# Kernel optimization log

Hardware: AMD Instinct MI355X
Metric: run time of the kernel (lower is better)

## Reference

```python
import jax, jax.numpy as jnp
import numpy as np

N_NODES = 100000
N_EDGES = 1600000
IN_DIM = 128
OUT_DIM = 64
N_HEADS = 4
NEG_SLOPE = 0.2
EPS = 1e-8


def setup_inputs() -> dict:
    key = jax.random.key(0)
    ks = jax.random.split(key, 6)
    x = jax.random.normal(ks[0], (N_NODES, IN_DIM), dtype=jnp.float32)
    edge_index = jax.random.randint(ks[1], (2, N_EDGES), 0, N_NODES, dtype=jnp.int64)
    # Xavier-uniform-ish init for linear weights, torch layout [out, in]
    bound = float(np.sqrt(6.0 / (IN_DIM + OUT_DIM)))
    Wq = jax.random.uniform(ks[2], (N_HEADS, OUT_DIM, IN_DIM), jnp.float32, -bound, bound)
    Wk = jax.random.uniform(ks[3], (N_HEADS, OUT_DIM, IN_DIM), jnp.float32, -bound, bound)
    Wh = jax.random.uniform(ks[4], (N_HEADS, OUT_DIM, IN_DIM), jnp.float32, -bound, bound)
    bh = jax.random.uniform(ks[5], (N_HEADS, OUT_DIM), jnp.float32, -bound, bound)
    return {"x": x, "edge_index": edge_index, "Wq": Wq, "Wk": Wk, "Wh": Wh, "bh": bh}


def reference(x, edge_index, Wq, Wk, Wh, bh):
    n_nodes = x.shape[0]
    row, col = edge_index[0], edge_index[1]
    n_heads = Wq.shape[0]
    scale = Wq.shape[1] ** 0.5
    outs = []
    for h in range(n_heads):  # fixed small head count; params differ per head
        Q = x @ Wq[h].T                                   # [N, out]
        K = x @ Wk[h].T                                   # [N, out]
        q_i = jax.nn.leaky_relu(Q[row], NEG_SLOPE)        # [E, out]
        k_j = jax.nn.leaky_relu(K[col], NEG_SLOPE)        # [E, out]
        scores = jnp.sum(q_i * k_j, axis=1) / scale       # [E]
        m = jax.ops.segment_max(scores, row, num_segments=n_nodes)
        e = jnp.exp(scores - m[row])
        z = jax.ops.segment_sum(e, row, num_segments=n_nodes)
        alpha = e / (z[row] + EPS)                        # [E]
        h_j = (x @ Wh[h].T + bh[h])[col]                  # [E, out]
        outs.append(jax.ops.segment_sum(alpha[:, None] * h_j, row, num_segments=n_nodes))
    return jnp.mean(jnp.stack(outs, axis=0), axis=0)      # [N, out]
```

## Files before the change

kernel.cpp:

```cpp
#include <hip/hip_runtime.h>
#include <math.h>

#define NIN 128
#define NOUT 64
#define FEAT 256
#define KHROW 512

typedef __attribute__((ext_vector_type(8))) short short8;
typedef __attribute__((ext_vector_type(4))) float f32x4;

__device__ __forceinline__ unsigned short f2bf(float f) {
    unsigned u = __float_as_uint(f);
    u = (u + 0x7FFFu + ((u >> 16) & 1u)) >> 16;
    return (unsigned short)u;
}
__device__ __forceinline__ float bflo(unsigned u) {
    return __uint_as_float(u << 16);
}
__device__ __forceinline__ float bfhi(unsigned u) {
    return __uint_as_float(u & 0xffff0000u);
}

__global__ __launch_bounds__(256) void wconv_kernel(
    const float* __restrict__ Wq, const float* __restrict__ Wk,
    const float* __restrict__ Wh, unsigned short* __restrict__ Wsw)
{
    const int id = blockIdx.x * 256 + threadIdx.x;
    const int lane = id & 63;
    const int kb   = (id >> 6) & 3;
    const int tile = (id >> 8) & 3;
    const int head = (id >> 10) & 3;
    const int mat  = id >> 12;
    const float* src = (mat == 0) ? Wq : (mat == 1) ? Wk : Wh;
    const int row   = tile * 16 + (lane & 15);
    const int kbase = kb * 32 + (lane >> 4) * 8;
    const float* sp = src + (size_t)(head * 64 + row) * NIN + kbase;
    const float4 a = *(const float4*)sp;
    const float4 b = *(const float4*)(sp + 4);
    uint4 w;
    w.x = (unsigned)f2bf(a.x) | ((unsigned)f2bf(a.y) << 16);
    w.y = (unsigned)f2bf(a.z) | ((unsigned)f2bf(a.w) << 16);
    w.z = (unsigned)f2bf(b.x) | ((unsigned)f2bf(b.y) << 16);
    w.w = (unsigned)f2bf(b.z) | ((unsigned)f2bf(b.w) << 16);
    *(uint4*)(Wsw + (size_t)id * 8) = w;
}

__global__ __launch_bounds__(256) void gemm_mfma_kernel(
    const float* __restrict__ x, const unsigned short* __restrict__ Wsw,
    const float* __restrict__ bh,
    unsigned short* __restrict__ QL, unsigned short* __restrict__ KH, int N,
    const int* __restrict__ ei, int E, int* __restrict__ deg,
    int* __restrict__ epos, int GB)
{
    if (blockIdx.x >= GB) {
        for (int e = (blockIdx.x - GB) * 256 + threadIdx.x; e < E; e += 512 * 256)
            epos[e] = atomicAdd(&deg[ei[e]], 1);
        return;
    }

    __shared__ char smem[34816];
    unsigned short (*xs)[136] = (unsigned short (*)[136])smem;

    const int nb = blockIdx.x * 128;
    const int t  = threadIdx.x;
    const int w  = t >> 6;
    const int l  = t & 63;

    #pragma unroll
    for (int j = 0; j < 16; ++j) {
        const int idx = j * 256 + t;
        const int row = idx >> 5;
        const int c4  = idx & 31;
        float4 xv = make_float4(0.f, 0.f, 0.f, 0.f);
        if (nb + row < N)
            xv = *(const float4*)(x + (size_t)(nb + row) * NIN + c4 * 4);
        ushort4 pk;
        pk.x = f2bf(xv.x); pk.y = f2bf(xv.y); pk.z = f2bf(xv.z); pk.w = f2bf(xv.w);
        *(ushort4*)(&xs[row][c4 * 4]) = pk;
    }
    __syncthreads();

    short8 bfrx[2][4];
    #pragma unroll
    for (int ns = 0; ns < 2; ++ns)
        #pragma unroll
        for (int kb = 0; kb < 4; ++kb)
            bfrx[ns][kb] = *(const short8*)(
                &xs[w * 32 + ns * 16 + (l & 15)][kb * 32 + (l >> 4) * 8]);
    __syncthreads();

    char* const sbw = smem + w * 4608;
    unsigned short* const wl = (unsigned short*)(smem + 18432);
    const int fsub = (l >> 4) * 4;

    for (int g = 0; g < 12; ++g) {
        const int mat  = g >> 2;
        const int head = g & 3;

        {
            const uint4* gw = (const uint4*)(Wsw + (size_t)g * 8192);
            uint4* wl4 = (uint4*)wl;
            #pragma unroll
            for (int j = 0; j < 4; ++j)
                wl4[j * 256 + t] = gw[j * 256 + t];
        }
        __syncthreads();

        #pragma unroll
        for (int tile = 0; tile < 4; ++tile) {
            f32x4 a0 = (f32x4){0.f, 0.f, 0.f, 0.f};
            f32x4 a1 = (f32x4){0.f, 0.f, 0.f, 0.f};
            #pragma unroll
            for (int kb = 0; kb < 4; ++kb) {
                const short8 afrw = *(const short8*)(
                    wl + (((tile * 4 + kb) << 9) + (l << 3)));
                a0 = __builtin_amdgcn_mfma_f32_16x16x32_bf16(afrw, bfrx[0][kb], a0, 0, 0, 0);
                a1 = __builtin_amdgcn_mfma_f32_16x16x32_bf16(afrw, bfrx[1][kb], a1, 0, 0, 0);
            }
            #pragma unroll
            for (int ns = 0; ns < 2; ++ns) {
                const f32x4 av = ns ? a1 : a0;
                float v0 = av[0], v1 = av[1], v2 = av[2], v3 = av[3];
                const int node = (l & 15) + ns * 16;
                if (mat == 2) {
                    const float4 bv = *(const float4*)(bh + head * NOUT + tile * 16 + fsub);
                    v0 += bv.x; v1 += bv.y; v2 += bv.z; v3 += bv.w;
                } else {
                    v0 = (v0 > 0.f) ? v0 : 0.2f * v0;
                    v1 = (v1 > 0.f) ? v1 : 0.2f * v1;
                    v2 = (v2 > 0.f) ? v2 : 0.2f * v2;
                    v3 = (v3 > 0.f) ? v3 : 0.2f * v3;
                }
                uint2 pk;
                pk.x = (unsigned)f2bf(v0) | ((unsigned)f2bf(v1) << 16);
                pk.y = (unsigned)f2bf(v2) | ((unsigned)f2bf(v3) << 16);
                *(uint2*)(sbw + node * 144 + (tile * 16 + fsub) * 2) = pk;
            }
        }

        #pragma unroll
        for (int jj = 0; jj < 4; ++jj) {
            const int node  = (l >> 3) + jj * 8;
            const int gnode = nb + w * 32 + node;
            const uint4 v = *(const uint4*)(sbw + node * 144 + (l & 7) * 16);
            if (gnode < N) {
                char* ob;
                if (mat == 0)      ob = (char*)QL + (size_t)gnode * 512 + head * 128;
                else if (mat == 1) ob = (char*)KH + (size_t)gnode * 1024 + head * 128;
                else               ob = (char*)KH + (size_t)gnode * 1024 + 512 + head * 128;
                *(uint4*)(ob + (l & 7) * 16) = v;
            }
        }
        __syncthreads();
    }
}

__global__ __launch_bounds__(1024) void bsum_kernel(const int* __restrict__ deg, int N,
                                                    int* __restrict__ bsum)
{
    __shared__ int wsum[16];
    const int t = threadIdx.x;
    const int idx = blockIdx.x * 1024 + t;
    int v = (idx < N) ? deg[idx] : 0;
    #pragma unroll
    for (int off = 1; off < 64; off <<= 1) v += __shfl_xor(v, off);
    if ((t & 63) == 0) wsum[t >> 6] = v;
    __syncthreads();
    if (t < 16) {
        int s = wsum[t];
        #pragma unroll
        for (int off = 1; off < 16; off <<= 1) s += __shfl_xor(s, off);
        if (t == 0) bsum[blockIdx.x] = s;
    }
}

__global__ __launch_bounds__(1024) void bscan_kernel(int* __restrict__ bsum, int NB,
                                                     int* __restrict__ rowstart, int N)
{
    __shared__ int wsum[16];
    const int t = threadIdx.x, lane = t & 63, wid = t >> 6;
    const int v = (t < NB) ? bsum[t] : 0;
    int s = v;
    #pragma unroll
    for (int off = 1; off < 64; off <<= 1) {
        int u = __shfl_up(s, off);
        if (lane >= off) s += u;
    }
    if (lane == 63) wsum[wid] = s;
    __syncthreads();
    if (wid == 0 && lane < 16) {
        int ss = wsum[lane];
        #pragma unroll
        for (int off = 1; off < 16; off <<= 1) {
            int u = __shfl_up(ss, off);
            if (lane >= off) ss += u;
        }
        wsum[lane] = ss;
    }
    __syncthreads();
    const int woff = (wid == 0) ? 0 : wsum[wid - 1];
    if (t < NB) bsum[t] = s + woff - v;
    if (t == 1023) rowstart[N] = s + woff;
}

__global__ __launch_bounds__(1024) void scan_apply_kernel(
    const int* __restrict__ deg, const int* __restrict__ bsum, int N,
    int* __restrict__ rowstart)
{
    __shared__ int wsum[16];
    const int t = threadIdx.x, lane = t & 63, wid = t >> 6;
    const int idx = blockIdx.x * 1024 + t;
    const int v = (idx < N) ? deg[idx] : 0;
    int s = v;
    #pragma unroll
    for (int off = 1; off < 64; off <<= 1) {
        int u = __shfl_up(s, off);
        if (lane >= off) s += u;
    }
    if (lane == 63) wsum[wid] = s;
    __syncthreads();
    if (wid == 0 && lane < 16) {
        int ss = wsum[lane];
        #pragma unroll
        for (int off = 1; off < 16; off <<= 1) {
            int u = __shfl_up(ss, off);
            if (lane >= off) ss += u;
        }
        wsum[lane] = ss;
    }
    __syncthreads();
    const int woff = (wid == 0) ? 0 : wsum[wid - 1];
    if (idx < N) rowstart[idx] = s + woff - v + bsum[blockIdx.x];
}

__global__ __launch_bounds__(256) void fill_kernel(const int* __restrict__ ei, int E,
                                                   const int* __restrict__ rowstart,
                                                   const int* __restrict__ epos,
                                                   int* __restrict__ csr_col)
{
    const int e = blockIdx.x * 256 + threadIdx.x;
    if (e < E)
        csr_col[rowstart[ei[e]] + epos[e]] = ei[E + e];
}

__global__ __launch_bounds__(256) void attn_kernel(
    const unsigned short* __restrict__ QL, const unsigned short* __restrict__ KH,
    const int* __restrict__ rowstart, const int* __restrict__ csr_col,
    float* __restrict__ out, int base, int N)
{
    const int n = base + blockIdx.x * 4 + (threadIdx.x >> 6);
    if (n >= N) return;
    const int l  = threadIdx.x & 63;
    const int g  = l >> 4;
    const int koff = ((l >> 2) & 3) * 64 + (l & 3) * 16;

    float qf[16];
    {
        const uint4* qp = (const uint4*)(QL + (size_t)n * FEAT + koff);
        const uint4 q0 = qp[0], q1 = qp[1];
        unsigned qs[8] = {q0.x, q0.y, q0.z, q0.w, q1.x, q1.y, q1.z, q1.w};
        #pragma unroll
        for (int tt = 0; tt < 8; ++tt) {
            qf[2 * tt]     = bflo(qs[tt]);
            qf[2 * tt + 1] = bfhi(qs[tt]);
        }
    }

    const int s0 = rowstart[n];
    const int s1 = rowstart[n + 1];

    float acc[16];
    #pragma unroll
    for (int j = 0; j < 16; ++j) acc[j] = 0.f;
    float z = 0.f;

    for (int i = s0; i < s1; i += 4) {
        const int eidx = i + g;
        if (eidx < s1) {
            const int c = csr_col[eidx];
            const uint4* kp = (const uint4*)(KH + (size_t)c * KHROW + koff);
            const uint4 k0 = kp[0],  k1 = kp[1];
            const uint4 h0 = kp[32], h1 = kp[33];

            unsigned ks[8] = {k0.x, k0.y, k0.z, k0.w, k1.x, k1.y, k1.z, k1.w};
            float p = 0.f;
            #pragma unroll
            for (int tt = 0; tt < 8; ++tt) {
                p = fmaf(qf[2 * tt],     bflo(ks[tt]), p);
                p = fmaf(qf[2 * tt + 1], bfhi(ks[tt]), p);
            }
            p += __shfl_xor(p, 1);
            p += __shfl_xor(p, 2);

            const float e = __expf(p * 0.125f);
            z += e;
            unsigned hs[8] = {h0.x, h0.y, h0.z, h0.w, h1.x, h1.y, h1.z, h1.w};
            #pragma unroll
            for (int tt = 0; tt < 8; ++tt) {
                acc[2 * tt]     = fmaf(e, bflo(hs[tt]), acc[2 * tt]);
                acc[2 * tt + 1] = fmaf(e, bfhi(hs[tt]), acc[2 * tt + 1]);
            }
        }
    }

    z += __shfl_xor(z, 16);
    z += __shfl_xor(z, 32);
    #pragma unroll
    for (int j = 0; j < 16; ++j) {
        acc[j] += __shfl_xor(acc[j], 16);
        acc[j] += __shfl_xor(acc[j], 32);
    }
    const float inv = 0.25f / (z + 1e-8f);
    #pragma unroll
    for (int j = 0; j < 16; ++j) {
        float r = acc[j] * inv;
        r += __shfl_xor(r, 4);
        r += __shfl_xor(r, 8);
        acc[j] = r;
    }
    if (l < 4) {
        float* ob = out + (size_t)n * NOUT + l * 16;
        *(float4*)(ob + 0)  = make_float4(acc[0],  acc[1],  acc[2],  acc[3]);
        *(float4*)(ob + 4)  = make_float4(acc[4],  acc[5],  acc[6],  acc[7]);
        *(float4*)(ob + 8)  = make_float4(acc[8],  acc[9],  acc[10], acc[11]);
        *(float4*)(ob + 12) = make_float4(acc[12], acc[13], acc[14], acc[15]);
    }
}

extern "C" void kernel_launch(void* const* d_in, const int* in_sizes, int n_in,
                              void* d_out, int out_size, void* d_ws, size_t ws_size,
                              hipStream_t stream)
{
    const float* x  = (const float*)d_in[0];
    const int*   ei = (const int*)d_in[1];
    const float* Wq = (const float*)d_in[2];
    const float* Wk = (const float*)d_in[3];
    const float* Wh = (const float*)d_in[4];
    const float* bh = (const float*)d_in[5];
    float* out = (float*)d_out;
    const int N = in_sizes[0] / NIN;
    const int E = in_sizes[1] / 2;

    char* p = (char*)d_ws;
    auto alloc = [&](size_t bytes) {
        char* r = p;
        p += (bytes + 255) & ~(size_t)255;
        return r;
    };
    unsigned short* QL  = (unsigned short*)alloc((size_t)N * FEAT * 2);
    unsigned short* KH  = (unsigned short*)alloc((size_t)N * KHROW * 2);
    unsigned short* Wsw = (unsigned short*)alloc((size_t)12288 * 8 * 2);
    int* deg      = (int*)alloc((size_t)N * 4);
    int* rowstart = (int*)alloc((size_t)(N + 1) * 4);
    int* epos     = (int*)alloc((size_t)E * 4);
    int* csr_col  = (int*)alloc((size_t)(E + 8) * 4);
    int* bsum     = (int*)alloc((size_t)1024 * 4);

    const int NB = (N + 1023) / 1024;
    const int GB = (N + 127) / 128;

    hipMemsetAsync(deg, 0, (size_t)N * 4, stream);

    wconv_kernel<<<48, 256, 0, stream>>>(Wq, Wk, Wh, Wsw);
    gemm_mfma_kernel<<<GB + 512, 256, 0, stream>>>(x, Wsw, bh, QL, KH, N,
                                                   ei, E, deg, epos, GB);
    bsum_kernel<<<NB, 1024, 0, stream>>>(deg, N, bsum);
    bscan_kernel<<<1, 1024, 0, stream>>>(bsum, NB, rowstart, N);
    scan_apply_kernel<<<NB, 1024, 0, stream>>>(deg, bsum, N, rowstart);
    fill_kernel<<<(E + 255) / 256, 256, 0, stream>>>(ei, E, rowstart, epos, csr_col);

    const int B1 = (N + 7) / 8;
    const int Btot = (N + 3) / 4;
    const int B2 = Btot - B1;
    attn_kernel<<<B1, 256, 0, stream>>>(QL, KH, rowstart, csr_col, out, 0, N);
    attn_kernel<<<B2, 256, 0, stream>>>(QL, KH, rowstart, csr_col, out, B1 * 4, N);
}
```

Measured before the change: 357.8 us.

## Split attention into two head-pair passes with head-pair-interleaved K/H layout

Reorders the KH buffer so each node's row holds K and H for heads 0-1 in the first 512 bytes and heads 2-3 in the second 512 bytes. The attention kernel is then launched twice, once per head pair, over all nodes. Each lane now loads one uint4 of K and one of H per edge instead of two of each, so every pass gathers only half of each neighbour row and the per-pass working set is smaller, which should help cache hit rates on the random gathers. The cost is that csr_col and rowstart are read twice, and the second pass has to read back the first pass's partial output and average it.

```diff
diff --git a/kernel.cpp b/kernel.cpp
--- a/kernel.cpp
+++ b/kernel.cpp
@@ -145,9 +145,13 @@
             const uint4 v = *(const uint4*)(sbw + node * 144 + (l & 7) * 16);
             if (gnode < N) {
                 char* ob;
-                if (mat == 0)      ob = (char*)QL + (size_t)gnode * 512 + head * 128;
-                else if (mat == 1) ob = (char*)KH + (size_t)gnode * 1024 + head * 128;
-                else               ob = (char*)KH + (size_t)gnode * 1024 + 512 + head * 128;
+                if (mat == 0) {
+                    ob = (char*)QL + (size_t)gnode * 512 + head * 128;
+                } else {
+                    const int pb = (head >> 1) * 512 + (head & 1) * 128
+                                 + (mat == 2 ? 256 : 0);
+                    ob = (char*)KH + (size_t)gnode * 1024 + pb;
+                }
                 *(uint4*)(ob + (l & 7) * 16) = v;
             }
         }
@@ -246,21 +250,24 @@
 __global__ __launch_bounds__(256) void attn_kernel(
     const unsigned short* __restrict__ QL, const unsigned short* __restrict__ KH,
     const int* __restrict__ rowstart, const int* __restrict__ csr_col,
-    float* __restrict__ out, int base, int N)
-{
-    const int n = base + blockIdx.x * 4 + (threadIdx.x >> 6);
+    float* __restrict__ out, int N, int hp)
+{
+    const int n = blockIdx.x * 4 + (threadIdx.x >> 6);
     if (n >= N) return;
     const int l  = threadIdx.x & 63;
     const int g  = l >> 4;
-    const int koff = ((l >> 2) & 3) * 64 + (l & 3) * 16;
-
-    float qf[16];
+    const int h2 = (l >> 3) & 1;
+    const int dr = l & 7;
+    const int kboff = hp * 512 + h2 * 128 + dr * 16;
+    const int hboff = kboff + 256;
+
+    float qf[8];
     {
-        const uint4* qp = (const uint4*)(QL + (size_t)n * FEAT + koff);
-        const uint4 q0 = qp[0], q1 = qp[1];
-        unsigned qs[8] = {q0.x, q0.y, q0.z, q0.w, q1.x, q1.y, q1.z, q1.w};
-        #pragma unroll
-        for (int tt = 0; tt < 8; ++tt) {
+        const uint4 qv = *(const uint4*)(QL + (size_t)n * FEAT
+                                         + (hp * 2 + h2) * 64 + dr * 8);
+        unsigned qs[4] = {qv.x, qv.y, qv.z, qv.w};
+        #pragma unroll
+        for (int tt = 0; tt < 4; ++tt) {
             qf[2 * tt]     = bflo(qs[tt]);
             qf[2 * tt + 1] = bfhi(qs[tt]);
         }
@@ -269,34 +276,35 @@
     const int s0 = rowstart[n];
     const int s1 = rowstart[n + 1];
 
-    float acc[16];
-    #pragma unroll
-    for (int j = 0; j < 16; ++j) acc[j] = 0.f;
+    float acc[8];
+    #pragma unroll
+    for (int j = 0; j < 8; ++j) acc[j] = 0.f;
     float z = 0.f;
 
     for (int i = s0; i < s1; i += 4) {
         const int eidx = i + g;
         if (eidx < s1) {
             const int c = csr_col[eidx];
-            const uint4* kp = (const uint4*)(KH + (size_t)c * KHROW + koff);
-            const uint4 k0 = kp[0],  k1 = kp[1];
-            const uint4 h0 = kp[32], h1 = kp[33];
-
-            unsigned ks[8] = {k0.x, k0.y, k0.z, k0.w, k1.x, k1.y, k1.z, k1.w};
+            const char* base = (const char*)KH + (size_t)c * 1024;
+            const uint4 ku = *(const uint4*)(base + kboff);
+            const uint4 hu = *(const uint4*)(base + hboff);
+
+            unsigned ks[4] = {ku.x, ku.y, ku.z, ku.w};
             float p = 0.f;
             #pragma unroll
-            for (int tt = 0; tt < 8; ++tt) {
+            for (int tt = 0; tt < 4; ++tt) {
                 p = fmaf(qf[2 * tt],     bflo(ks[tt]), p);
                 p = fmaf(qf[2 * tt + 1], bfhi(ks[tt]), p);
             }
             p += __shfl_xor(p, 1);
             p += __shfl_xor(p, 2);
+            p += __shfl_xor(p, 4);
 
             const float e = __expf(p * 0.125f);
             z += e;
-            unsigned hs[8] = {h0.x, h0.y, h0.z, h0.w, h1.x, h1.y, h1.z, h1.w};
-            #pragma unroll
-            for (int tt = 0; tt < 8; ++tt) {
+            unsigned hs[4] = {hu.x, hu.y, hu.z, hu.w};
+            #pragma unroll
+            for (int tt = 0; tt < 4; ++tt) {
                 acc[2 * tt]     = fmaf(e, bflo(hs[tt]), acc[2 * tt]);
                 acc[2 * tt + 1] = fmaf(e, bfhi(hs[tt]), acc[2 * tt + 1]);
             }
@@ -306,24 +314,34 @@
     z += __shfl_xor(z, 16);
     z += __shfl_xor(z, 32);
     #pragma unroll
-    for (int j = 0; j < 16; ++j) {
+    for (int j = 0; j < 8; ++j) {
         acc[j] += __shfl_xor(acc[j], 16);
         acc[j] += __shfl_xor(acc[j], 32);
     }
-    const float inv = 0.25f / (z + 1e-8f);
-    #pragma unroll
-    for (int j = 0; j < 16; ++j) {
+    const float inv = 1.f / (z + 1e-8f);
+    #pragma unroll
+    for (int j = 0; j < 8; ++j) {
         float r = acc[j] * inv;
-        r += __shfl_xor(r, 4);
         r += __shfl_xor(r, 8);
         acc[j] = r;
     }
-    if (l < 4) {
-        float* ob = out + (size_t)n * NOUT + l * 16;
-        *(float4*)(ob + 0)  = make_float4(acc[0],  acc[1],  acc[2],  acc[3]);
-        *(float4*)(ob + 4)  = make_float4(acc[4],  acc[5],  acc[6],  acc[7]);
-        *(float4*)(ob + 8)  = make_float4(acc[8],  acc[9],  acc[10], acc[11]);
-        *(float4*)(ob + 12) = make_float4(acc[12], acc[13], acc[14], acc[15]);
+    if (l < 8) {
+        float* ob = out + (size_t)n * NOUT + l * 8;
+        if (hp == 0) {
+            *(float4*)(ob + 0) = make_float4(acc[0], acc[1], acc[2], acc[3]);
+            *(float4*)(ob + 4) = make_float4(acc[4], acc[5], acc[6], acc[7]);
+        } else {
+            const float4 p0 = *(const float4*)(ob + 0);
+            const float4 p1 = *(const float4*)(ob + 4);
+            *(float4*)(ob + 0) = make_float4((p0.x + acc[0]) * 0.25f,
+                                             (p0.y + acc[1]) * 0.25f,
+                                             (p0.z + acc[2]) * 0.25f,
+                                             (p0.w + acc[3]) * 0.25f);
+            *(float4*)(ob + 4) = make_float4((p1.x + acc[4]) * 0.25f,
+                                             (p1.y + acc[5]) * 0.25f,
+                                             (p1.z + acc[6]) * 0.25f,
+                                             (p1.w + acc[7]) * 0.25f);
+        }
     }
 }
 
@@ -369,9 +387,7 @@
     scan_apply_kernel<<<NB, 1024, 0, stream>>>(deg, bsum, N, rowstart);
     fill_kernel<<<(E + 255) / 256, 256, 0, stream>>>(ei, E, rowstart, epos, csr_col);
 
-    const int B1 = (N + 7) / 8;
-    const int Btot = (N + 3) / 4;
-    const int B2 = Btot - B1;
-    attn_kernel<<<B1, 256, 0, stream>>>(QL, KH, rowstart, csr_col, out, 0, N);
-    attn_kernel<<<B2, 256, 0, stream>>>(QL, KH, rowstart, csr_col, out, B1 * 4, N);
-}
+    const int AB = (N + 3) / 4;
+    attn_kernel<<<AB, 256, 0, stream>>>(QL, KH, rowstart, csr_col, out, N, 0);
+    attn_kernel<<<AB, 256, 0, stream>>>(QL, KH, rowstart, csr_col, out, N, 1);
+}
```

New measurement: 357.3 us (median of 2 runs). No clear change (-0.1%).
